# Optimization experiments

Hardware: AMD Instinct MI355X
Metric: run time of the kernel (lower is better)

## Reference

```python
import jax, jax.numpy as jnp
import numpy as np

B, C, H, W = 4, 128, 64, 64


def setup_inputs() -> dict:
    key = jax.random.key(0)
    ks = jax.random.split(key, 7)
    s = 1.0 / np.sqrt(C)  # torch Conv2d default init scale (uniform bound)
    x = jax.random.normal(ks[0], (B, C, H, W), dtype=jnp.float32)
    Wq = jax.random.uniform(ks[1], (C, C), jnp.float32, -s, s)
    bq = jax.random.uniform(ks[2], (C,), jnp.float32, -s, s)
    Wk = jax.random.uniform(ks[3], (C, C), jnp.float32, -s, s)
    bk = jax.random.uniform(ks[4], (C,), jnp.float32, -s, s)
    Wv = jax.random.uniform(ks[5], (C, C), jnp.float32, -s, s)
    bv = jax.random.uniform(ks[6], (C,), jnp.float32, -s, s)
    return {"x": x, "Wq": Wq, "bq": bq, "Wk": Wk, "bk": bk, "Wv": Wv, "bv": bv}


def _conv1x1_flat(x_flat, Wt, b):
    # x_flat: [B, C, N]; 1x1 conv == channel matmul
    return jnp.einsum('oc,bcn->bon', Wt, x_flat) + b[None, :, None]


def reference(x, Wq, bq, Wk, bk, Wv, bv):
    b_, c_, h_, w_ = x.shape
    n = h_ * w_
    xf = x.reshape(b_, c_, n)
    k_map = _conv1x1_flat(xf, Wk, bk)              # [B, C, N]
    q_map = _conv1x1_flat(xf, Wq, bq)              # [B, C, N]
    v_map = _conv1x1_flat(xf, Wv, bv)              # [B, C, N]
    energy = jnp.einsum('bci,bcj->bij', q_map, k_map)   # [B, N, N]
    attention = jax.nn.softmax(energy, axis=-1)
    # out[b,c,i] = sum_j v[b,c,j] * attention[b,i,j]  (v @ attention^T)
    out = jnp.einsum('bcj,bij->bci', v_map, attention)  # [B, C, N]
    return x + out.reshape(b_, c_, h_, w_)
```

## Files before the change

kernel.cpp:

```cpp
#include <hip/hip_runtime.h>

#define B_ 4
#define C_ 128
#define N_ 4096
#define LOG2E 1.44269504088896340736f
#define KB_PER_B (C_ * N_ * 2)

typedef __bf16 bf16x8 __attribute__((ext_vector_type(8)));
typedef __bf16 bf16x4 __attribute__((ext_vector_type(4)));
typedef float  f32x16 __attribute__((ext_vector_type(16)));
typedef int    i32x4  __attribute__((ext_vector_type(4)));
typedef int    i32x2  __attribute__((ext_vector_type(2)));

static __device__ __forceinline__ void stage16(const void* g_lane, char* lds_base, int lane16) {
#if __has_builtin(__builtin_amdgcn_global_load_lds)
    __builtin_amdgcn_global_load_lds(
        (const __attribute__((address_space(1))) void*)g_lane,
        (__attribute__((address_space(3))) void*)lds_base, 16, 0, 0);
    (void)lane16;
#else
    *(i32x4*)(lds_base + lane16) = *(const i32x4*)g_lane;
#endif
}

__global__ __launch_bounds__(256) void proj_kernel(
    const float* __restrict__ x,
    const float* __restrict__ Wq, const float* __restrict__ bq,
    const float* __restrict__ Wk, const float* __restrict__ bk,
    const float* __restrict__ Wv, const float* __restrict__ bv,
    unsigned short* __restrict__ qT, char* __restrict__ kQ,
    char* __restrict__ vQ)
{
    __shared__ __align__(16) char wlds[32768];

    const int tid  = threadIdx.x;
    const int wave = tid >> 6;
    const int lane = tid & 63;
    const int col  = lane & 31;
    const int h    = lane >> 5;

    const int jw  = blockIdx.x * 4 + wave;
    const int mat = jw >> 9;
    const int rem = jw & 511;
    const int b   = rem >> 7;
    const int nb  = rem & 127;
    const int n   = nb * 32 + col;

    const float* W    = (mat == 0) ? Wq : (mat == 1) ? Wk : Wv;
    const float* bias = (mat == 0) ? bq : (mat == 1) ? bk : bv;
    const float  scale = (mat == 0) ? LOG2E : 1.0f;

    #pragma unroll
    for (int k = 0; k < 16; ++k) {
        const int q = tid + k * 256;
        const int o = q >> 5;
        const int g = q & 31;
        float4 w = *((const float4*)W + q);
        bf16x4 d;
        d[0] = (__bf16)(w.x * scale); d[1] = (__bf16)(w.y * scale);
        d[2] = (__bf16)(w.z * scale); d[3] = (__bf16)(w.w * scale);
        *(bf16x4*)(wlds + o * 256 + ((((g >> 1) ^ (o & 15)) << 4) | ((g & 1) * 8))) = d;
    }
    __syncthreads();

    bf16x8 xf[8];
    const float* xcol = x + (size_t)b * C_ * N_ + n;
    #pragma unroll
    for (int ch = 0; ch < 8; ++ch) {
        const int c0 = ch * 16 + 8 * h;
        bf16x8 v;
        #pragma unroll
        for (int e = 0; e < 8; ++e) v[e] = (__bf16)xcol[(size_t)(c0 + e) * N_];
        xf[ch] = v;
    }

    f32x16 acc[4];
    #pragma unroll
    for (int ob = 0; ob < 4; ++ob)
        #pragma unroll
        for (int rr = 0; rr < 16; ++rr) acc[ob][rr] = 0.0f;

    #pragma unroll
    for (int ch = 0; ch < 8; ++ch) {
        #pragma unroll
        for (int ob = 0; ob < 4; ++ob) {
            const char* wrow = wlds + (ob * 32 + col) * 256;
            bf16x8 wf = __builtin_bit_cast(bf16x8,
                *(const i32x4*)(wrow + (((ch * 2 + h) ^ (col & 15)) << 4)));
            acc[ob] = __builtin_amdgcn_mfma_f32_32x32x16_bf16(
                wf, xf[ch], acc[ob], 0, 0, 0);
        }
    }

    if (mat == 0) {
        unsigned short* dst = qT + (size_t)(b * N_ + n) * C_;
        #pragma unroll
        for (int ob = 0; ob < 4; ++ob) {
            #pragma unroll
            for (int qd = 0; qd < 4; ++qd) {
                const int obase = ob * 32 + 8 * qd + 4 * h;
                bf16x4 d;
                d[0] = (__bf16)(acc[ob][4 * qd + 0] + bias[obase + 0] * scale);
                d[1] = (__bf16)(acc[ob][4 * qd + 1] + bias[obase + 1] * scale);
                d[2] = (__bf16)(acc[ob][4 * qd + 2] + bias[obase + 2] * scale);
                d[3] = (__bf16)(acc[ob][4 * qd + 3] + bias[obase + 3] * scale);
                *(bf16x4*)(dst + obase) = d;
            }
        }
    } else if (mat == 1) {
        const int kt = (nb & 1) * 32 + col;
        char* dst = kQ + (size_t)b * KB_PER_B + (size_t)(nb >> 1) * 16384 + kt * 256;
        const int kx = kt & 15;
        #pragma unroll
        for (int ob = 0; ob < 4; ++ob) {
            #pragma unroll
            for (int qd = 0; qd < 4; ++qd) {
                const int obase = ob * 32 + 8 * qd + 4 * h;
                bf16x4 d;
                d[0] = (__bf16)(acc[ob][4 * qd + 0] + bias[obase + 0]);
                d[1] = (__bf16)(acc[ob][4 * qd + 1] + bias[obase + 1]);
                d[2] = (__bf16)(acc[ob][4 * qd + 2] + bias[obase + 2]);
                d[3] = (__bf16)(acc[ob][4 * qd + 3] + bias[obase + 3]);
                *(bf16x4*)(dst + ((((ob * 4 + qd) ^ kx) << 4) | (8 * h))) = d;
            }
        }
    } else {
        char* dst = vQ + (size_t)b * KB_PER_B + (size_t)(nb >> 1) * 16384;
        const int kt  = (nb & 1) * 32 + col;
        const int m   = kt >> 4;
        const int w16 = kt & 15;
        const int hk  = (w16 >> 2) & 1;
        const int pos = (w16 & 3) | (((w16 >> 3) & 1) << 2);
        #pragma unroll
        for (int ob = 0; ob < 4; ++ob) {
            #pragma unroll
            for (int rr = 0; rr < 16; ++rr) {
                const int o = ob * 32 + (rr & 3) + 8 * (rr >> 2) + 4 * h;
                const int R = o >> 1;
                const int cidx = (o & 1) * 8 + 2 * m + hk;
                *(unsigned short*)(dst + R * 256 + (((cidx ^ (R & 15)) << 4)) + pos * 2) =
                    __builtin_bit_cast(unsigned short,
                                       (__bf16)(acc[ob][rr] + bias[o]));
            }
        }
    }
}

template<int NS>
__global__ __launch_bounds__(256, 2) void attn_kernel(
    const unsigned short* __restrict__ qT,
    const char* __restrict__ kQ,
    const char* __restrict__ vQ,
    unsigned short* __restrict__ pO,
    float2* __restrict__ mlG)
{
    __shared__ __align__(16) char smem[65536];

    const int tid  = threadIdx.x;
    const int w    = tid >> 6;
    const int lane = tid & 63;
    const int l31  = lane & 31;
    const int h    = lane >> 5;

    const int orig = blockIdx.x;
    const int b    = (orig & 7) >> 1;
    const int idx  = ((orig >> 3) << 1) | (orig & 1);
    const int quarter = idx % NS;
    const int qg   = idx / NS;
    const int i0   = qg * 128 + w * 32;

    const int NT = N_ / (NS * 64);
    const char* kq0 = kQ + (size_t)b * KB_PER_B + (size_t)(quarter * NT) * 16384;
    const char* vq0 = vQ + (size_t)b * KB_PER_B + (size_t)(quarter * NT) * 16384;

    bf16x8 qf[8];
    {
        const unsigned short* qrow = qT + (size_t)(b * N_ + i0 + l31) * C_;
        #pragma unroll
        for (int ch = 0; ch < 8; ++ch)
            qf[ch] = __builtin_bit_cast(bf16x8, *(const i32x4*)(qrow + ch * 16 + 8 * h));
    }
    bf16x8 ones;
    #pragma unroll
    for (int e = 0; e < 8; ++e) ones[e] = (__bf16)1.0f;

    f32x16 accO[4];
    #pragma unroll
    for (int cb = 0; cb < 4; ++cb)
        #pragma unroll
        for (int rr = 0; rr < 16; ++rr) accO[cb][rr] = 0.0f;
    f32x16 ls;
    #pragma unroll
    for (int rr = 0; rr < 16; ++rr) ls[rr] = 0.0f;
    float m_run = -1e30f;

    const int lane16 = lane * 16;
    auto stage = [&](int t, char* buf) {
        const char* g = ((w < 2) ? kq0 : vq0) + (size_t)t * 16384 + (w & 1) * 8192 + lane16;
        char* d = buf + (w >> 1) * 16384 + (w & 1) * 8192;
        #pragma unroll
        for (int u = 0; u < 8; ++u)
            stage16(g + u * 1024, d + u * 1024, lane16);
    };

    stage(0, smem);
    __syncthreads();
    int cur = 0;

    #pragma unroll 1
    for (int t = 0; t < NT; ++t) {
        char* kb = smem + cur * 32768;
        char* vb = kb + 16384;
        if (t + 1 < NT) stage(t + 1, smem + (cur ^ 1) * 32768);

        f32x16 e0, e1;
        #pragma unroll
        for (int rr = 0; rr < 16; ++rr) { e0[rr] = 0.0f; e1[rr] = 0.0f; }
        {
            const char* kr0 = kb + l31 * 256;
            const int   kx  = l31 & 15;
            __builtin_amdgcn_s_setprio(1);
            #pragma unroll
            for (int ch = 0; ch < 8; ++ch) {
                const int off = ((2 * ch + h) ^ kx) << 4;
                bf16x8 k0 = __builtin_bit_cast(bf16x8, *(const i32x4*)(kr0 + off));
                e0 = __builtin_amdgcn_mfma_f32_32x32x16_bf16(k0, qf[ch], e0, 0, 0, 0);
                bf16x8 k1 = __builtin_bit_cast(bf16x8, *(const i32x4*)(kr0 + 8192 + off));
                e1 = __builtin_amdgcn_mfma_f32_32x32x16_bf16(k1, qf[ch], e1, 0, 0, 0);
            }
            __builtin_amdgcn_s_setprio(0);
        }

        float a[8];
        #pragma unroll
        for (int i = 0; i < 8; ++i)
            a[i] = fmaxf(fmaxf(e0[2 * i], e0[2 * i + 1]),
                         fmaxf(e1[2 * i], e1[2 * i + 1]));
        float mt = fmaxf(fmaxf(fmaxf(a[0], a[1]), fmaxf(a[2], a[3])),
                         fmaxf(fmaxf(a[4], a[5]), fmaxf(a[6], a[7])));
        mt = fmaxf(mt, __shfl_xor(mt, 32, 64));
        if (!__all(mt <= m_run + 8.0f)) {
            const float mn = fmaxf(m_run, mt);
            const float sc = exp2f(m_run - mn);
            #pragma unroll
            for (int cb = 0; cb < 4; ++cb)
                #pragma unroll
                for (int rr = 0; rr < 16; ++rr) accO[cb][rr] *= sc;
            #pragma unroll
            for (int rr = 0; rr < 16; ++rr) ls[rr] *= sc;
            m_run = mn;
        }
        #pragma unroll
        for (int rr = 0; rr < 16; ++rr) {
            e0[rr] = exp2f(e0[rr] - m_run);
            e1[rr] = exp2f(e1[rr] - m_run);
        }

        bf16x8 pf[4];
        #pragma unroll
        for (int m = 0; m < 4; ++m) {
            bf16x8 p;
            #pragma unroll
            for (int e = 0; e < 8; ++e)
                p[e] = (__bf16)((m < 2) ? e0[(m & 1) * 8 + e] : e1[(m & 1) * 8 + e]);
            pf[m] = p;
        }

        __builtin_amdgcn_s_setprio(1);
        #pragma unroll
        for (int m = 0; m < 4; ++m)
            ls = __builtin_amdgcn_mfma_f32_32x32x16_bf16(ones, pf[m], ls, 0, 0, 0);
        {
            const int rsw = l31 >> 1;
            const int ci  = (l31 & 1) * 8;
            #pragma unroll
            for (int cb = 0; cb < 4; ++cb) {
                const char* vrow = vb + (cb * 16 + (l31 >> 1)) * 256;
                #pragma unroll
                for (int m = 0; m < 4; ++m) {
                    bf16x8 vf = __builtin_bit_cast(bf16x8,
                        *(const i32x4*)(vrow + (((ci + 2 * m + h) ^ rsw) << 4)));
                    accO[cb] = __builtin_amdgcn_mfma_f32_32x32x16_bf16(
                        vf, pf[m], accO[cb], 0, 0, 0);
                }
            }
        }
        __builtin_amdgcn_s_setprio(0);

        __syncthreads();
        cur ^= 1;
    }

    const float l_run = ls[0];
    if (h == 0)
        mlG[((size_t)quarter * B_ + b) * N_ + i0 + l31] = make_float2(m_run, l_run);

    unsigned short* pOq = pO + ((size_t)quarter * B_ + b) * C_ * N_;
    #pragma unroll
    for (int cb = 0; cb < 4; ++cb) {
        #pragma unroll
        for (int rr = 0; rr < 16; ++rr) {
            const int c = cb * 32 + (rr & 3) + 8 * (rr >> 2) + 4 * h;
            pOq[(size_t)c * N_ + i0 + l31] =
                __builtin_bit_cast(unsigned short, (__bf16)accO[cb][rr]);
        }
    }
}

template<int NS>
__global__ __launch_bounds__(256) void merge_kernel(
    const float* __restrict__ x,
    const unsigned short* __restrict__ pO,
    const float2* __restrict__ mlG,
    float* __restrict__ out)
{
    const int idx = blockIdx.x * 256 + threadIdx.x;
    const int nq  = idx & (N_ / 4 - 1);
    const int bc  = idx >> 10;
    const int b   = bc >> 7;
    const size_t off = (size_t)bc * N_ + nq * 4;

    float4 xv = *(const float4*)(x + off);

    float2 ml[NS][4];
    #pragma unroll
    for (int q = 0; q < NS; ++q) {
        const float2* mp = mlG + ((size_t)q * B_ + b) * N_ + nq * 4;
        #pragma unroll
        for (int j = 0; j < 4; ++j) ml[q][j] = mp[j];
    }
    float M[4];
    #pragma unroll
    for (int j = 0; j < 4; ++j) {
        M[j] = ml[0][j].x;
        #pragma unroll
        for (int q = 1; q < NS; ++q) M[j] = fmaxf(M[j], ml[q][j].x);
    }
    float num[4] = {0, 0, 0, 0}, den[4] = {0, 0, 0, 0};
    #pragma unroll
    for (int q = 0; q < NS; ++q) {
        bf16x4 r = *(const bf16x4*)(pO + (size_t)q * B_ * C_ * N_ + off);
        #pragma unroll
        for (int j = 0; j < 4; ++j) {
            float wq = exp2f(ml[q][j].x - M[j]);
            num[j] += wq * (float)r[j];
            den[j] += wq * ml[q][j].y;
        }
    }
    float4 ov;
    ov.x = xv.x + num[0] / den[0];
    ov.y = xv.y + num[1] / den[1];
    ov.z = xv.z + num[2] / den[2];
    ov.w = xv.w + num[3] / den[3];
    *(float4*)(out + off) = ov;
}

extern "C" void kernel_launch(void* const* d_in, const int* in_sizes, int n_in,
                              void* d_out, int out_size, void* d_ws, size_t ws_size,
                              hipStream_t stream)
{
    const float* x  = (const float*)d_in[0];
    const float* Wq = (const float*)d_in[1];
    const float* bq = (const float*)d_in[2];
    const float* Wk = (const float*)d_in[3];
    const float* bk = (const float*)d_in[4];
    const float* Wv = (const float*)d_in[5];
    const float* bv = (const float*)d_in[6];
    float* out = (float*)d_out;

    unsigned short* qT = (unsigned short*)d_ws;
    char* kQ = (char*)(qT + (size_t)B_ * N_ * C_);
    char* vQ = kQ + (size_t)B_ * KB_PER_B;
    unsigned short* pO = (unsigned short*)(vQ + (size_t)B_ * KB_PER_B);

    const size_t slotO  = (size_t)B_ * C_ * N_;
    const size_t slotML = (size_t)B_ * N_;
    const size_t need4  = 3ull * B_ * N_ * C_ * 2 + 4 * (slotO * 2 + slotML * 8);

    proj_kernel<<<384, 256, 0, stream>>>(x, Wq, bq, Wk, bk, Wv, bv, qT, kQ, vQ);

    if (ws_size >= need4) {
        float2* mlG = (float2*)(pO + 4 * slotO);
        attn_kernel<4><<<B_ * (N_ / 128) * 4, 256, 0, stream>>>(qT, kQ, vQ, pO, mlG);
        merge_kernel<4><<<(B_ * C_ * N_ / 4) / 256, 256, 0, stream>>>(x, pO, mlG, out);
    } else {
        float2* mlG = (float2*)(pO + 2 * slotO);
        attn_kernel<2><<<B_ * (N_ / 128) * 2, 256, 0, stream>>>(qT, kQ, vQ, pO, mlG);
        merge_kernel<2><<<(B_ * C_ * N_ / 4) / 256, 256, 0, stream>>>(x, pO, mlG, out);
    }
}
```

Before: 72.31 us.

## Halve KV tile to 32 keys, raise occupancy, add 8-way key split

Shrinks the per-iteration key/value tile from 64 to 32 keys and relays out the K and V workspace to match, with a narrower V row and a reduced swizzle. This halves LDS per block so three blocks can share a CU, and the smaller accumulator set eases register pressure. A new 8-way split-K path runs when workspace allows, giving more blocks. The cost is more loop iterations and barriers per key, and a larger partial-output write and merge pass.

```diff
diff --git a/kernel.cpp b/kernel.cpp
--- a/kernel.cpp
+++ b/kernel.cpp
@@ -10,7 +10,6 @@
 typedef __bf16 bf16x4 __attribute__((ext_vector_type(4)));
 typedef float  f32x16 __attribute__((ext_vector_type(16)));
 typedef int    i32x4  __attribute__((ext_vector_type(4)));
-typedef int    i32x2  __attribute__((ext_vector_type(2)));
 
 static __device__ __forceinline__ void stage16(const void* g_lane, char* lds_base, int lane16) {
 #if __has_builtin(__builtin_amdgcn_global_load_lds)
@@ -108,9 +107,8 @@
             }
         }
     } else if (mat == 1) {
-        const int kt = (nb & 1) * 32 + col;
-        char* dst = kQ + (size_t)b * KB_PER_B + (size_t)(nb >> 1) * 16384 + kt * 256;
-        const int kx = kt & 15;
+        char* dst = kQ + (size_t)b * KB_PER_B + (size_t)nb * 8192 + col * 256;
+        const int kx = col & 15;
         #pragma unroll
         for (int ob = 0; ob < 4; ++ob) {
             #pragma unroll
@@ -125,10 +123,9 @@
             }
         }
     } else {
-        char* dst = vQ + (size_t)b * KB_PER_B + (size_t)(nb >> 1) * 16384;
-        const int kt  = (nb & 1) * 32 + col;
-        const int m   = kt >> 4;
-        const int w16 = kt & 15;
+        char* dst = vQ + (size_t)b * KB_PER_B + (size_t)nb * 8192;
+        const int m   = col >> 4;
+        const int w16 = col & 15;
         const int hk  = (w16 >> 2) & 1;
         const int pos = (w16 & 3) | (((w16 >> 3) & 1) << 2);
         #pragma unroll
@@ -137,8 +134,8 @@
             for (int rr = 0; rr < 16; ++rr) {
                 const int o = ob * 32 + (rr & 3) + 8 * (rr >> 2) + 4 * h;
                 const int R = o >> 1;
-                const int cidx = (o & 1) * 8 + 2 * m + hk;
-                *(unsigned short*)(dst + R * 256 + (((cidx ^ (R & 15)) << 4)) + pos * 2) =
+                const int cidx = (o & 1) * 4 + 2 * m + hk;
+                *(unsigned short*)(dst + R * 128 + ((cidx ^ (R & 7)) << 4) + pos * 2) =
                     __builtin_bit_cast(unsigned short,
                                        (__bf16)(acc[ob][rr] + bias[o]));
             }
@@ -147,14 +144,14 @@
 }
 
 template<int NS>
-__global__ __launch_bounds__(256, 2) void attn_kernel(
+__global__ __launch_bounds__(256, 3) void attn_kernel(
     const unsigned short* __restrict__ qT,
     const char* __restrict__ kQ,
     const char* __restrict__ vQ,
     unsigned short* __restrict__ pO,
     float2* __restrict__ mlG)
 {
-    __shared__ __align__(16) char smem[65536];
+    __shared__ __align__(16) char smem[32768];
 
     const int tid  = threadIdx.x;
     const int w    = tid >> 6;
@@ -165,13 +162,13 @@
     const int orig = blockIdx.x;
     const int b    = (orig & 7) >> 1;
     const int idx  = ((orig >> 3) << 1) | (orig & 1);
-    const int quarter = idx % NS;
+    const int part = idx % NS;
     const int qg   = idx / NS;
     const int i0   = qg * 128 + w * 32;
 
-    const int NT = N_ / (NS * 64);
-    const char* kq0 = kQ + (size_t)b * KB_PER_B + (size_t)(quarter * NT) * 16384;
-    const char* vq0 = vQ + (size_t)b * KB_PER_B + (size_t)(quarter * NT) * 16384;
+    const int NT = N_ / (NS * 32);
+    const char* kq0 = kQ + (size_t)b * KB_PER_B + (size_t)(part * NT) * 8192;
+    const char* vq0 = vQ + (size_t)b * KB_PER_B + (size_t)(part * NT) * 8192;
 
     bf16x8 qf[8];
     {
@@ -196,10 +193,10 @@
 
     const int lane16 = lane * 16;
     auto stage = [&](int t, char* buf) {
-        const char* g = ((w < 2) ? kq0 : vq0) + (size_t)t * 16384 + (w & 1) * 8192 + lane16;
-        char* d = buf + (w >> 1) * 16384 + (w & 1) * 8192;
-        #pragma unroll
-        for (int u = 0; u < 8; ++u)
+        const char* g = ((w < 2) ? kq0 : vq0) + (size_t)t * 8192 + (w & 1) * 4096 + lane16;
+        char* d = buf + (w >> 1) * 8192 + (w & 1) * 4096;
+        #pragma unroll
+        for (int u = 0; u < 4; ++u)
             stage16(g + u * 1024, d + u * 1024, lane16);
     };
 
@@ -209,35 +206,31 @@
 
     #pragma unroll 1
     for (int t = 0; t < NT; ++t) {
-        char* kb = smem + cur * 32768;
-        char* vb = kb + 16384;
-        if (t + 1 < NT) stage(t + 1, smem + (cur ^ 1) * 32768);
-
-        f32x16 e0, e1;
-        #pragma unroll
-        for (int rr = 0; rr < 16; ++rr) { e0[rr] = 0.0f; e1[rr] = 0.0f; }
+        char* kb = smem + cur * 16384;
+        char* vb = kb + 8192;
+        if (t + 1 < NT) stage(t + 1, smem + (cur ^ 1) * 16384);
+
+        f32x16 e;
+        #pragma unroll
+        for (int rr = 0; rr < 16; ++rr) e[rr] = 0.0f;
         {
-            const char* kr0 = kb + l31 * 256;
-            const int   kx  = l31 & 15;
+            const char* kr = kb + l31 * 256;
+            const int   kx = l31 & 15;
             __builtin_amdgcn_s_setprio(1);
             #pragma unroll
             for (int ch = 0; ch < 8; ++ch) {
-                const int off = ((2 * ch + h) ^ kx) << 4;
-                bf16x8 k0 = __builtin_bit_cast(bf16x8, *(const i32x4*)(kr0 + off));
-                e0 = __builtin_amdgcn_mfma_f32_32x32x16_bf16(k0, qf[ch], e0, 0, 0, 0);
-                bf16x8 k1 = __builtin_bit_cast(bf16x8, *(const i32x4*)(kr0 + 8192 + off));
-                e1 = __builtin_amdgcn_mfma_f32_32x32x16_bf16(k1, qf[ch], e1, 0, 0, 0);
+                bf16x8 kf = __builtin_bit_cast(bf16x8,
+                    *(const i32x4*)(kr + (((2 * ch + h) ^ kx) << 4)));
+                e = __builtin_amdgcn_mfma_f32_32x32x16_bf16(kf, qf[ch], e, 0, 0, 0);
             }
             __builtin_amdgcn_s_setprio(0);
         }
 
-        float a[8];
-        #pragma unroll
-        for (int i = 0; i < 8; ++i)
-            a[i] = fmaxf(fmaxf(e0[2 * i], e0[2 * i + 1]),
-                         fmaxf(e1[2 * i], e1[2 * i + 1]));
-        float mt = fmaxf(fmaxf(fmaxf(a[0], a[1]), fmaxf(a[2], a[3])),
-                         fmaxf(fmaxf(a[4], a[5]), fmaxf(a[6], a[7])));
+        float a0 = fmaxf(fmaxf(e[0], e[1]), fmaxf(e[2], e[3]));
+        float a1 = fmaxf(fmaxf(e[4], e[5]), fmaxf(e[6], e[7]));
+        float a2 = fmaxf(fmaxf(e[8], e[9]), fmaxf(e[10], e[11]));
+        float a3 = fmaxf(fmaxf(e[12], e[13]), fmaxf(e[14], e[15]));
+        float mt = fmaxf(fmaxf(a0, a1), fmaxf(a2, a3));
         mt = fmaxf(mt, __shfl_xor(mt, 32, 64));
         if (!__all(mt <= m_run + 8.0f)) {
             const float mn = fmaxf(m_run, mt);
@@ -251,33 +244,28 @@
             m_run = mn;
         }
         #pragma unroll
-        for (int rr = 0; rr < 16; ++rr) {
-            e0[rr] = exp2f(e0[rr] - m_run);
-            e1[rr] = exp2f(e1[rr] - m_run);
-        }
-
-        bf16x8 pf[4];
-        #pragma unroll
-        for (int m = 0; m < 4; ++m) {
+        for (int rr = 0; rr < 16; ++rr) e[rr] = exp2f(e[rr] - m_run);
+
+        bf16x8 pf[2];
+        #pragma unroll
+        for (int m = 0; m < 2; ++m) {
             bf16x8 p;
             #pragma unroll
-            for (int e = 0; e < 8; ++e)
-                p[e] = (__bf16)((m < 2) ? e0[(m & 1) * 8 + e] : e1[(m & 1) * 8 + e]);
+            for (int ee = 0; ee < 8; ++ee) p[ee] = (__bf16)e[m * 8 + ee];
             pf[m] = p;
         }
 
         __builtin_amdgcn_s_setprio(1);
-        #pragma unroll
-        for (int m = 0; m < 4; ++m)
-            ls = __builtin_amdgcn_mfma_f32_32x32x16_bf16(ones, pf[m], ls, 0, 0, 0);
+        ls = __builtin_amdgcn_mfma_f32_32x32x16_bf16(ones, pf[0], ls, 0, 0, 0);
+        ls = __builtin_amdgcn_mfma_f32_32x32x16_bf16(ones, pf[1], ls, 0, 0, 0);
         {
-            const int rsw = l31 >> 1;
-            const int ci  = (l31 & 1) * 8;
+            const int rsw = (l31 >> 1) & 7;
+            const int ci  = (l31 & 1) * 4;
             #pragma unroll
             for (int cb = 0; cb < 4; ++cb) {
-                const char* vrow = vb + (cb * 16 + (l31 >> 1)) * 256;
+                const char* vrow = vb + (cb * 16 + (l31 >> 1)) * 128;
                 #pragma unroll
-                for (int m = 0; m < 4; ++m) {
+                for (int m = 0; m < 2; ++m) {
                     bf16x8 vf = __builtin_bit_cast(bf16x8,
                         *(const i32x4*)(vrow + (((ci + 2 * m + h) ^ rsw) << 4)));
                     accO[cb] = __builtin_amdgcn_mfma_f32_32x32x16_bf16(
@@ -291,11 +279,10 @@
         cur ^= 1;
     }
 
-    const float l_run = ls[0];
     if (h == 0)
-        mlG[((size_t)quarter * B_ + b) * N_ + i0 + l31] = make_float2(m_run, l_run);
-
-    unsigned short* pOq = pO + ((size_t)quarter * B_ + b) * C_ * N_;
+        mlG[((size_t)part * B_ + b) * N_ + i0 + l31] = make_float2(m_run, ls[0]);
+
+    unsigned short* pOq = pO + ((size_t)part * B_ + b) * C_ * N_;
     #pragma unroll
     for (int cb = 0; cb < 4; ++cb) {
         #pragma unroll
@@ -375,17 +362,24 @@
 
     const size_t slotO  = (size_t)B_ * C_ * N_;
     const size_t slotML = (size_t)B_ * N_;
-    const size_t need4  = 3ull * B_ * N_ * C_ * 2 + 4 * (slotO * 2 + slotML * 8);
+    const size_t base   = 3ull * B_ * N_ * C_ * 2;
+    const size_t need8  = base + 8 * (slotO * 2 + slotML * 8);
+    const size_t need4  = base + 4 * (slotO * 2 + slotML * 8);
+    const int nMerge = (B_ * C_ * N_ / 4) / 256;
 
     proj_kernel<<<384, 256, 0, stream>>>(x, Wq, bq, Wk, bk, Wv, bv, qT, kQ, vQ);
 
-    if (ws_size >= need4) {
+    if (ws_size >= need8) {
+        float2* mlG = (float2*)(pO + 8 * slotO);
+        attn_kernel<8><<<B_ * (N_ / 128) * 8, 256, 0, stream>>>(qT, kQ, vQ, pO, mlG);
+        merge_kernel<8><<<nMerge, 256, 0, stream>>>(x, pO, mlG, out);
+    } else if (ws_size >= need4) {
         float2* mlG = (float2*)(pO + 4 * slotO);
         attn_kernel<4><<<B_ * (N_ / 128) * 4, 256, 0, stream>>>(qT, kQ, vQ, pO, mlG);
-        merge_kernel<4><<<(B_ * C_ * N_ / 4) / 256, 256, 0, stream>>>(x, pO, mlG, out);
+        merge_kernel<4><<<nMerge, 256, 0, stream>>>(x, pO, mlG, out);
     } else {
         float2* mlG = (float2*)(pO + 2 * slotO);
         attn_kernel<2><<<B_ * (N_ / 128) * 2, 256, 0, stream>>>(qT, kQ, vQ, pO, mlG);
-        merge_kernel<2><<<(B_ * C_ * N_ / 4) / 256, 256, 0, stream>>>(x, pO, mlG, out);
-    }
-}
+        merge_kernel<2><<<nMerge, 256, 0, stream>>>(x, pO, mlG, out);
+    }
+}
```

Result: slower. 84.11 us (+16.3%).
